# Kernel optimization log

Hardware: AMD Instinct MI355X
Metric: run time of the kernel (lower is better)

Reference implementation:

```python
import jax, jax.numpy as jnp
import numpy as np

N = 2048       # x_dim (input features)
M = 2048       # y_dim (output features)
R0 = 1024      # components in table 0 (knn table)
D_K = 1024     # key encoder embed dim
D_V = 1024     # val encoder embed dim
BATCH = 512
ISTA_ALPHA = 1.0
ISTA_MAXITER = 5


def _ortho_encoder(key, n, d):
    # get_embedding_matrix with ortho=True: QR of (s,s) gaussian, take [:n,:d]
    s = max(n, d)
    q = jnp.linalg.qr(jax.random.normal(key, (s, s), dtype=jnp.float32))[0]
    return q[:n, :d]


def setup_inputs() -> dict:
    key = jax.random.key(0)
    kw, kk, kv, kx = jax.random.split(key, 4)
    W = jax.random.normal(kw, (N, M), dtype=jnp.float32) / np.float32(np.sqrt(N))
    # torch: V, S, U = svd(W); U = U.T  -> V = left vecs (n,k), U = right vecs (m,k)
    Usvd, S, Vh = jnp.linalg.svd(W, full_matrices=False)
    V = Usvd          # (n, k)
    Ur = Vh.T         # (m, k)
    key_enc = _ortho_encoder(kk, N, D_K)   # (n, d_k)
    val_enc = _ortho_encoder(kv, M, D_V)   # (m, d_v)
    # table 0: knn table over components [0:R0]
    keys_t0 = V[:, :R0].T @ key_enc        # (R0, d_k)
    vals_t0 = Ur[:, :R0].T @ val_enc       # (R0, d_v)
    scales_t0 = S[:R0][:, None]            # (R0, 1)
    # table 1: plain low-rank table over components [R0:]
    keys_t1 = V[:, R0:]                    # (n, R1)
    vals_t1 = Ur[:, R0:]                   # (m, R1)
    scales_t1 = S[R0:][:, None]            # (R1, 1)
    x = jax.random.normal(kx, (BATCH, N), dtype=jnp.float32)
    return {"x": x, "key_enc": key_enc, "val_enc": val_enc,
            "keys_t0": keys_t0, "vals_t0": vals_t0, "scales_t0": scales_t0,
            "keys_t1": keys_t1, "vals_t1": vals_t1, "scales_t1": scales_t1}


def _soft(x, t):
    return jnp.sign(x) * jnp.maximum(jnp.abs(x) - t, 0.0)


def reference(x, key_enc, val_enc, keys_t0, vals_t0, scales_t0,
              keys_t1, vals_t1, scales_t1):
    # --- table 0: knn path (batched; original looped over batch samples) ---
    q = x @ key_enc                        # (B, d_k)
    alphas = q @ keys_t0.T                 # (B, R0)
    betas = alphas * scales_t0.T           # (B, R0)
    yb = betas @ vals_t0                   # (B, d_v)
    # ISTA: min ||yb - z @ val_enc||^2 + alpha*||z||_1, step=1 (val_enc has
    # orthonormal columns so Lipschitz const of grad is 1)
    z = yb @ val_enc.T                     # z0, (B, m)
    for _ in range(ISTA_MAXITER):
        z = _soft(z + (yb - z @ val_enc) @ val_enc.T, ISTA_ALPHA)
    y = z                                  # knn path assigns y[b,:] = yh
    # --- table 1: low-rank path (accumulates) ---
    alphas2 = x @ keys_t1                  # (B, R1)
    betas2 = alphas2 * scales_t1.T         # (B, R1)
    y = y + betas2 @ vals_t1.T             # (B, m)
    return y
```

## Files before the change

kernel.cpp:

```cpp
#include <hip/hip_runtime.h>


typedef _Float16 f16x8 __attribute__((ext_vector_type(8)));
typedef _Float16 f16x4 __attribute__((ext_vector_type(4)));
typedef float f32x4 __attribute__((ext_vector_type(4)));

enum { EPI_H, EPI_QOFF, EPI_SPLIT, EPI_SOFT, EPI_ZQ, EPI_ZQF, EPI_FINAL };

typedef const __attribute__((address_space(1))) void* gas_ptr;
typedef __attribute__((address_space(3))) void* las_ptr;

__device__ __forceinline__ void gload16(const void* g, void* l) {
  __builtin_amdgcn_global_load_lds((gas_ptr)g, (las_ptr)l, 16, 0, 0);
}

__device__ __forceinline__ float softt(float t) {
  float s = fabsf(t) - 1.0f;
  s = s > 0.0f ? s : 0.0f;
  return copysignf(s, t);
}

__global__ __launch_bounds__(256) void convAll(
    const float* __restrict__ e0, const float* __restrict__ e1,
    const float* __restrict__ e2, const float* __restrict__ e3,
    _Float16* __restrict__ o0, _Float16* __restrict__ o1,
    _Float16* __restrict__ o2, _Float16* __restrict__ o3,
    const float* __restrict__ s1, const float* __restrict__ s2,
    const float4* __restrict__ pa, f16x4* __restrict__ qa, int na,
    const float4* __restrict__ pb, f16x4* __restrict__ qb, int nb,
    const float4* __restrict__ pc, f16x4* __restrict__ qc, int nc) {
  const int z = blockIdx.z;
  if (z == 4) {
    const int total = na + nb + nc;
    const int bid = blockIdx.y * 32 + blockIdx.x;
    const int nthr = 2048 * 256;
    for (int i = bid * 256 + threadIdx.y * 32 + threadIdx.x; i < total;
         i += nthr) {
      const float4* s;
      f16x4* d;
      int j = i;
      if (j < na) {
        s = pa; d = qa;
      } else if ((j -= na) < nb) {
        s = pb; d = qb;
      } else {
        j -= nb; s = pc; d = qc;
      }
      float4 v = s[j];
      f16x4 h = {(_Float16)v.x, (_Float16)v.y, (_Float16)v.z, (_Float16)v.w};
      d[j] = h;
    }
    return;
  }
  const float* in = z == 0 ? e0 : z == 1 ? e1 : z == 2 ? e2 : e3;
  _Float16* out = z == 0 ? o0 : z == 1 ? o1 : z == 2 ? o2 : o3;
  const int R = (z < 2) ? 2048 : 1024;
  const int C = 1024;
  const int mode = z == 1 ? 1 : z == 2 ? 2 : 0;
  const float* sv = z == 1 ? s1 : s2;
  __shared__ float t[32][33];
  const int tx = threadIdx.x, ty = threadIdx.y;
  const int c0 = blockIdx.x * 32, r0 = blockIdx.y * 32;
  if (r0 >= R) return;
#pragma unroll
  for (int i = 0; i < 32; i += 8)
    t[ty + i][tx] = in[(size_t)(r0 + ty + i) * C + c0 + tx];
  __syncthreads();
#pragma unroll
  for (int i = 0; i < 32; i += 8) {
    float v = t[tx][ty + i];
    if (mode == 1) v *= sv[c0 + ty + i];
    if (mode == 2) v *= sv[r0 + tx];
    out[(size_t)(c0 + ty + i) * R + r0 + tx] = (_Float16)v;
  }
}

template <int EPI>
__device__ __forceinline__ void gtile(
    const _Float16* __restrict__ A, int lda, const _Float16* __restrict__ B,
    int ldb, int nK, int N, int brow, int bcol, const float* __restrict__ dgv,
    float* __restrict__ dgout, float* __restrict__ fA, float* __restrict__ fB,
    _Float16* __restrict__ oh, _Float16* __restrict__ oh2,
    float* __restrict__ ofin, _Float16* sm, int tid) {
  const int lane = tid & 63;
  const int w = tid >> 6;
  const int wr = w & 1;
  const int wk = w >> 1;
  const int srow = lane >> 3;
  const int scol = ((lane & 7) ^ srow) << 3;
  const int a15 = lane & 15;
  const int hi = lane >> 4;
  const int l7 = lane & 7;

  const _Float16* apg = A + (size_t)(brow + (w << 4) + srow) * lda + scol;
  const _Float16* bpg = B + (size_t)(bcol + (w << 4) + srow) * ldb + scol;
  _Float16* AB = sm;
  _Float16* BB = sm + 16384;
  const int ldstA = w << 10;

  const int ca = ((wk << 2) + hi) ^ l7;
  int raddr[2], baddr[4];
#pragma unroll
  for (int mi = 0; mi < 2; ++mi)
    raddr[mi] = ((wr << 5) + (mi << 4) + a15) * 64 + (ca << 3);
#pragma unroll
  for (int ni = 0; ni < 4; ++ni)
    baddr[ni] = ((ni << 4) + a15) * 64 + (ca << 3);

  f32x4 acc[2][4] = {};

  __syncthreads();

#pragma unroll
  for (int p = 0; p < 2; ++p) {
    gload16(apg + p * 64, AB + p * 4096 + ldstA);
    gload16(apg + p * 64 + (size_t)8 * lda, AB + p * 4096 + ldstA + 512);
    gload16(bpg + p * 64, BB + p * 4096 + ldstA);
    gload16(bpg + p * 64 + (size_t)8 * ldb, BB + p * 4096 + ldstA + 512);
  }

  for (int kt = 0; kt < nK; ++kt) {
    if (kt + 2 < nK) {
      const int bf = (kt + 2) & 3;
      const int co = (kt + 2) << 6;
      gload16(apg + co, AB + bf * 4096 + ldstA);
      gload16(apg + co + (size_t)8 * lda, AB + bf * 4096 + ldstA + 512);
      gload16(bpg + co, BB + bf * 4096 + ldstA);
      gload16(bpg + co + (size_t)8 * ldb, BB + bf * 4096 + ldstA + 512);
    }
    const int rem = nK - 1 - kt;
    if (rem >= 2)
      asm volatile("s_waitcnt vmcnt(8)" ::: "memory");
    else if (rem == 1)
      asm volatile("s_waitcnt vmcnt(4)" ::: "memory");
    else
      asm volatile("s_waitcnt vmcnt(0)" ::: "memory");
    __builtin_amdgcn_s_barrier();
    __builtin_amdgcn_sched_barrier(0);
    const _Float16* Ab = AB + (kt & 3) * 4096;
    const _Float16* Bb = BB + (kt & 3) * 4096;
    f16x8 av[2], bv[4];
    av[0] = *(const f16x8*)(Ab + raddr[0]);
    av[1] = *(const f16x8*)(Ab + raddr[1]);
    bv[0] = *(const f16x8*)(Bb + baddr[0]);
    bv[1] = *(const f16x8*)(Bb + baddr[1]);
    bv[2] = *(const f16x8*)(Bb + baddr[2]);
    bv[3] = *(const f16x8*)(Bb + baddr[3]);
#pragma unroll
    for (int mi = 0; mi < 2; ++mi)
#pragma unroll
      for (int ni = 0; ni < 4; ++ni)
        acc[mi][ni] = __builtin_amdgcn_mfma_f32_16x16x32_f16(
            av[mi], bv[ni], acc[mi][ni], 0, 0, 0);
  }

  __syncthreads();
  float* scr = (float*)sm;
  const int sl = (wr << 6) + lane;
  if (wk == 1) {
#pragma unroll
    for (int mi = 0; mi < 2; ++mi)
#pragma unroll
      for (int ni = 0; ni < 4; ++ni)
#pragma unroll
        for (int r = 0; r < 4; ++r)
          scr[(((mi << 2) + ni) * 4 + r) * 128 + sl] = acc[mi][ni][r];
  }
  __syncthreads();
  if (wk == 0) {
#pragma unroll
    for (int mi = 0; mi < 2; ++mi) {
#pragma unroll
      for (int ni = 0; ni < 4; ++ni) {
#pragma unroll
        for (int r = 0; r < 4; ++r) {
          const float v =
              acc[mi][ni][r] + scr[(((mi << 2) + ni) * 4 + r) * 128 + sl];
          const int row = brow + (wr << 5) + (mi << 4) + (hi << 2) + r;
          const int col = bcol + (ni << 4) + a15;
          const size_t idx = (size_t)row * N + col;
          if constexpr (EPI == EPI_H) {
            oh[idx] = (_Float16)v;
          } else if constexpr (EPI == EPI_QOFF) {
            if (row == col) {
              dgout[row] = 1.0f - v;
              oh[idx] = (_Float16)0.0f;
            } else {
              oh[idx] = (_Float16)(-v);
            }
          } else if constexpr (EPI == EPI_SPLIT) {
            if (col < 1024)
              oh[(size_t)row * 1024 + col] = (_Float16)v;
            else
              oh2[(size_t)row * 1024 + (col - 1024)] = (_Float16)v;
          }
        }
      }
    }
  }
}

template <int EPI>
__device__ __forceinline__ void gt32(
    const _Float16* __restrict__ A, int lda, const _Float16* __restrict__ B,
    int ldb, int nK, int N, int brow, int bcol, const float* __restrict__ dgv,
    float* __restrict__ fA, float* __restrict__ fB,
    _Float16* __restrict__ oh, float* __restrict__ ofin, _Float16* sm,
    int tid) {
  const int lane = tid & 63;
  const int w = tid >> 6;
  const int wc = w & 1;
  const int wk = w >> 1;
  const int srow = lane >> 3;
  const int scol = ((lane & 7) ^ srow) << 3;
  const int a15 = lane & 15, hi = lane >> 4, l7 = lane & 7;

  const _Float16* apg = A + (size_t)(brow + (w << 3) + srow) * lda + scol;
  const _Float16* bpg = B + (size_t)(bcol + (w << 4) + srow) * ldb + scol;
  _Float16* AB = sm;
  _Float16* BB = sm + 8192;
  const int ca = ((wk << 2) + hi) ^ l7;
  int raddr[2], baddr[2];
#pragma unroll
  for (int mi = 0; mi < 2; ++mi)
    raddr[mi] = ((mi << 4) + a15) * 64 + (ca << 3);
#pragma unroll
  for (int ni = 0; ni < 2; ++ni)
    baddr[ni] = ((wc << 5) + (ni << 4) + a15) * 64 + (ca << 3);

  f32x4 acc[2][2] = {};
  __syncthreads();

#pragma unroll
  for (int p = 0; p < 2; ++p) {
    gload16(apg + p * 64, AB + p * 2048 + (w << 9));
    gload16(bpg + p * 64, BB + p * 4096 + (w << 10));
    gload16(bpg + p * 64 + (size_t)8 * ldb, BB + p * 4096 + (w << 10) + 512);
  }
  for (int kt = 0; kt < nK; ++kt) {
    if (kt + 2 < nK) {
      const int bf = (kt + 2) & 3;
      const int co = (kt + 2) << 6;
      gload16(apg + co, AB + bf * 2048 + (w << 9));
      gload16(bpg + co, BB + bf * 4096 + (w << 10));
      gload16(bpg + co + (size_t)8 * ldb, BB + bf * 4096 + (w << 10) + 512);
    }
    const int rem = nK - 1 - kt;
    if (rem >= 2)
      asm volatile("s_waitcnt vmcnt(6)" ::: "memory");
    else if (rem == 1)
      asm volatile("s_waitcnt vmcnt(3)" ::: "memory");
    else
      asm volatile("s_waitcnt vmcnt(0)" ::: "memory");
    __builtin_amdgcn_s_barrier();
    __builtin_amdgcn_sched_barrier(0);
    const _Float16* Ab = AB + (kt & 3) * 2048;
    const _Float16* Bb = BB + (kt & 3) * 4096;
    f16x8 av[2], bv[2];
    av[0] = *(const f16x8*)(Ab + raddr[0]);
    av[1] = *(const f16x8*)(Ab + raddr[1]);
    bv[0] = *(const f16x8*)(Bb + baddr[0]);
    bv[1] = *(const f16x8*)(Bb + baddr[1]);
#pragma unroll
    for (int mi = 0; mi < 2; ++mi)
#pragma unroll
      for (int ni = 0; ni < 2; ++ni)
        acc[mi][ni] = __builtin_amdgcn_mfma_f32_16x16x32_f16(
            av[mi], bv[ni], acc[mi][ni], 0, 0, 0);
  }
  __syncthreads();
  float* scr = (float*)sm;
  const int sl = (wc << 6) + lane;
  if (wk == 1) {
#pragma unroll
    for (int mi = 0; mi < 2; ++mi)
#pragma unroll
      for (int ni = 0; ni < 2; ++ni)
#pragma unroll
        for (int r = 0; r < 4; ++r)
          scr[(((mi << 1) + ni) * 4 + r) * 128 + sl] = acc[mi][ni][r];
  }
  __syncthreads();
  if (wk == 0) {
#pragma unroll
    for (int mi = 0; mi < 2; ++mi) {
#pragma unroll
      for (int ni = 0; ni < 2; ++ni) {
#pragma unroll
        for (int r = 0; r < 4; ++r) {
          const float v =
              acc[mi][ni][r] + scr[(((mi << 1) + ni) * 4 + r) * 128 + sl];
          const int row = brow + (mi << 4) + (hi << 2) + r;
          const int col = bcol + (wc << 5) + (ni << 4) + a15;
          const size_t idx = (size_t)row * N + col;
          if constexpr (EPI == EPI_SOFT) {
            fA[idx] = v;
            float s = softt(v);
            fB[idx] = s;
            oh[idx] = (_Float16)s;
          } else if constexpr (EPI == EPI_ZQ) {
            float t = fA[idx] + dgv[col] * fB[idx] + v;
            float s = softt(t);
            fB[idx] = s;
            oh[idx] = (_Float16)s;
          } else if constexpr (EPI == EPI_ZQF) {
            float t = fA[idx] + dgv[col] * fB[idx] + v;
            fB[idx] = softt(t);
          } else {
            ofin[idx] = fB[idx] + v;
          }
        }
      }
    }
  }
}

struct WS {
  const _Float16 *ve, *vt1, *w0pT_r, *Bcat, *qoff_r, *x, *kt0s, *vt0T, *w0_r,
      *q_r, *be2;
  _Float16 *w0pT_w, *qoff_w, *w0_w, *q_w, *be2_w, *zhA, *zhB;
  float *z0, *zf, *dg;
};

__device__ __forceinline__ void map512(int b, int& br, int& bc) {
  const int x = b & 7, i = b >> 3;
  bc = (x << 2) | (i & 3);
  br = i >> 2;
}

__global__ __launch_bounds__(256, 2) void kD2(WS p) {
  __shared__ __align__(16) _Float16 sm[32768];
  const int tid = threadIdx.x;
  const int bid = blockIdx.x;
  if (bid < 1024) {
    gtile<EPI_QOFF>(p.ve, 1024, p.ve, 1024, 16, 2048, (bid >> 5) << 6,
                    (bid & 31) << 6, nullptr, p.dg, nullptr, nullptr, p.qoff_w,
                    nullptr, nullptr, sm, tid);
  } else if (bid < 1280) {
    const int i = bid - 1024;
    gtile<EPI_SPLIT>(p.x, 2048, p.Bcat, 2048, 32, 2048, (i >> 5) << 6,
                     (i & 31) << 6, nullptr, nullptr, nullptr, nullptr, p.q_w,
                     p.be2_w, nullptr, sm, tid);
  } else {
    const int i = bid - 1280;
    gtile<EPI_H>(p.kt0s, 1024, p.vt0T, 1024, 16, 1024, (i >> 4) << 6,
                 (i & 15) << 6, nullptr, nullptr, nullptr, nullptr, p.w0_w,
                 nullptr, nullptr, sm, tid);
  }
}

__global__ __launch_bounds__(256, 2) void kW0p(WS p) {
  __shared__ __align__(16) _Float16 sm[32768];
  const int x = blockIdx.x & 7, i = blockIdx.x >> 3;
  const int bc = (x << 1) | (i & 1), br = i >> 1;
  gtile<EPI_H>(p.ve, 1024, p.w0_r, 1024, 16, 1024, br << 6, bc << 6, nullptr,
               nullptr, nullptr, nullptr, p.w0pT_w, nullptr, nullptr, sm,
               threadIdx.x);
}

__global__ __launch_bounds__(256, 2) void kC2(WS p) {
  __shared__ __align__(16) _Float16 sm[24576];
  int br, bc;
  map512(blockIdx.x, br, bc);
  gt32<EPI_SOFT>(p.q_r, 1024, p.w0pT_r, 1024, 16, 2048, br << 5, bc << 6,
                 nullptr, p.z0, p.zf, p.zhA, nullptr, sm, threadIdx.x);
}

template <bool AB>
__global__ __launch_bounds__(256, 2) void kZQ(WS p) {
  __shared__ __align__(16) _Float16 sm[24576];
  int br, bc;
  map512(blockIdx.x, br, bc);
  gt32<EPI_ZQ>(AB ? p.zhA : p.zhB, 2048, p.qoff_r, 2048, 32, 2048, br << 5,
               bc << 6, p.dg, p.z0, p.zf, AB ? p.zhB : p.zhA, nullptr, sm,
               threadIdx.x);
}

__global__ __launch_bounds__(256, 2) void kZQF(WS p, float* out) {
  __shared__ __align__(16) _Float16 sm[24576];
  int br, bc;
  map512(blockIdx.x, br, bc);
  gt32<EPI_ZQF>(p.zhB, 2048, p.qoff_r, 2048, 32, 2048, br << 5, bc << 6, p.dg,
                p.z0, p.zf, nullptr, nullptr, sm, threadIdx.x);
  gt32<EPI_FINAL>(p.be2, 1024, p.vt1, 1024, 16, 2048, br << 5, bc << 6,
                  nullptr, nullptr, p.zf, nullptr, out, sm, threadIdx.x);
}

extern "C" void kernel_launch(void* const* d_in, const int* in_sizes, int n_in,
                              void* d_out, int out_size, void* d_ws,
                              size_t ws_size, hipStream_t stream) {
  const float* x = (const float*)d_in[0];
  const float* key_enc = (const float*)d_in[1];
  const float* val_enc = (const float*)d_in[2];
  const float* keys_t0 = (const float*)d_in[3];
  const float* vals_t0 = (const float*)d_in[4];
  const float* scales_t0 = (const float*)d_in[5];
  const float* keys_t1 = (const float*)d_in[6];
  const float* vals_t1 = (const float*)d_in[7];
  const float* scales_t1 = (const float*)d_in[8];

  constexpr size_t M1 = 1048576;
  _Float16* ws = (_Float16*)d_ws;
  _Float16* ve_h = ws;
  _Float16* vt1_h = ws + 2 * M1;
  _Float16* w0pT = ws + 4 * M1;
  _Float16* Bcat = ws + 6 * M1;
  _Float16* zhA = ws + 6 * M1;
  float* z0_f = (float*)(ws + 7 * M1);
  _Float16* zhB = ws + 9 * M1;
  _Float16* qoff = ws + 10 * M1;
  _Float16* x_h = ws + 14 * M1;
  _Float16* kt0s = ws + 15 * M1;
  float* z_f = (float*)(ws + 15 * M1);
  _Float16* vt0T = ws + 16 * M1;
  _Float16* w0 = ws + 17 * M1;
  _Float16* q_h = ws + 18 * M1;
  _Float16* be2 = ws + 18 * M1 + 524288;
  float* dg = (float*)(ws + 19 * M1);

  WS p;
  p.ve = ve_h; p.vt1 = vt1_h; p.w0pT_r = w0pT; p.w0pT_w = w0pT;
  p.Bcat = Bcat; p.qoff_r = qoff; p.qoff_w = qoff; p.x = x_h;
  p.kt0s = kt0s; p.vt0T = vt0T; p.w0_r = w0; p.w0_w = w0;
  p.q_r = q_h; p.q_w = q_h; p.be2 = be2; p.be2_w = be2;
  p.zhA = zhA; p.zhB = zhB; p.z0 = z0_f; p.zf = z_f; p.dg = dg;

  convAll<<<dim3(32, 64, 5), dim3(32, 8), 0, stream>>>(
      key_enc, keys_t1, keys_t0, vals_t0, Bcat, Bcat + 2 * M1, kt0s, vt0T,
      scales_t1, scales_t0, (const float4*)x, (f16x4*)x_h, 262144,
      (const float4*)val_enc, (f16x4*)ve_h, 524288, (const float4*)vals_t1,
      (f16x4*)vt1_h, 524288);
  kD2<<<1536, 256, 0, stream>>>(p);
  kW0p<<<512, 256, 0, stream>>>(p);
  kC2<<<512, 256, 0, stream>>>(p);
  kZQ<true><<<512, 256, 0, stream>>>(p);
  kZQ<false><<<512, 256, 0, stream>>>(p);
  kZQ<true><<<512, 256, 0, stream>>>(p);
  kZQF<<<512, 256, 0, stream>>>(p, (float*)d_out);
}
```

Baseline: 110.3 us.

## Reassociate knn-table GEMM chain and deepen gt32 pipeline to three stages

```diff
diff --git a/kernel.cpp b/kernel.cpp
--- a/kernel.cpp
+++ b/kernel.cpp
@@ -21,67 +21,64 @@
 }
 
 __global__ __launch_bounds__(256) void convAll(
-    const float* __restrict__ e0, const float* __restrict__ e1,
-    const float* __restrict__ e2, const float* __restrict__ e3,
-    _Float16* __restrict__ o0, _Float16* __restrict__ o1,
-    _Float16* __restrict__ o2, _Float16* __restrict__ o3,
-    const float* __restrict__ s1, const float* __restrict__ s2,
-    const float4* __restrict__ pa, f16x4* __restrict__ qa, int na,
-    const float4* __restrict__ pb, f16x4* __restrict__ qb, int nb,
-    const float4* __restrict__ pc, f16x4* __restrict__ qc, int nc) {
-  const int z = blockIdx.z;
-  if (z == 4) {
-    const int total = na + nb + nc;
-    const int bid = blockIdx.y * 32 + blockIdx.x;
-    const int nthr = 2048 * 256;
-    for (int i = bid * 256 + threadIdx.y * 32 + threadIdx.x; i < total;
-         i += nthr) {
-      const float4* s;
-      f16x4* d;
-      int j = i;
-      if (j < na) {
-        s = pa; d = qa;
-      } else if ((j -= na) < nb) {
-        s = pb; d = qb;
-      } else {
-        j -= nb; s = pc; d = qc;
-      }
-      float4 v = s[j];
-      f16x4 h = {(_Float16)v.x, (_Float16)v.y, (_Float16)v.z, (_Float16)v.w};
-      d[j] = h;
+    const float* __restrict__ k1, _Float16* __restrict__ k1s1T,
+    const float* __restrict__ s1, const float* __restrict__ x,
+    _Float16* __restrict__ x_h, const float* __restrict__ ve,
+    _Float16* __restrict__ ve_h, const float* __restrict__ vt1,
+    _Float16* __restrict__ vt1_h, const float* __restrict__ k0,
+    _Float16* __restrict__ k0s, const float* __restrict__ s0,
+    const float* __restrict__ v0, _Float16* __restrict__ v0_h,
+    const float* __restrict__ ke, _Float16* __restrict__ ke_h) {
+  if (blockIdx.z == 0) {
+    __shared__ float t[32][33];
+    const int tx = threadIdx.x, ty = threadIdx.y;
+    const int c0 = blockIdx.x * 32, r0 = blockIdx.y * 32;
+#pragma unroll
+    for (int i = 0; i < 32; i += 8)
+      t[ty + i][tx] = k1[(size_t)(r0 + ty + i) * 1024 + c0 + tx];
+    __syncthreads();
+#pragma unroll
+    for (int i = 0; i < 32; i += 8) {
+      float v = t[tx][ty + i] * s1[c0 + ty + i];
+      k1s1T[(size_t)(c0 + ty + i) * 2048 + r0 + tx] = (_Float16)v;
     }
     return;
   }
-  const float* in = z == 0 ? e0 : z == 1 ? e1 : z == 2 ? e2 : e3;
-  _Float16* out = z == 0 ? o0 : z == 1 ? o1 : z == 2 ? o2 : o3;
-  const int R = (z < 2) ? 2048 : 1024;
-  const int C = 1024;
-  const int mode = z == 1 ? 1 : z == 2 ? 2 : 0;
-  const float* sv = z == 1 ? s1 : s2;
-  __shared__ float t[32][33];
-  const int tx = threadIdx.x, ty = threadIdx.y;
-  const int c0 = blockIdx.x * 32, r0 = blockIdx.y * 32;
-  if (r0 >= R) return;
-#pragma unroll
-  for (int i = 0; i < 32; i += 8)
-    t[ty + i][tx] = in[(size_t)(r0 + ty + i) * C + c0 + tx];
-  __syncthreads();
-#pragma unroll
-  for (int i = 0; i < 32; i += 8) {
-    float v = t[tx][ty + i];
-    if (mode == 1) v *= sv[c0 + ty + i];
-    if (mode == 2) v *= sv[r0 + tx];
-    out[(size_t)(c0 + ty + i) * R + r0 + tx] = (_Float16)v;
+  const int bid = blockIdx.y * 32 + blockIdx.x;
+  const int n_x = 262144, n_ve = 524288, n_v1 = 524288, n_k0 = 262144,
+            n_v0 = 262144, n_ke = 524288;
+  const int total = n_x + n_ve + n_v1 + n_k0 + n_v0 + n_ke;
+  for (int i = bid * 256 + threadIdx.y * 32 + threadIdx.x; i < total;
+       i += 2048 * 256) {
+    int j = i;
+    const float4* s;
+    f16x4* d;
+    float sc = 1.0f;
+    if (j < n_x) {
+      s = (const float4*)x; d = (f16x4*)x_h;
+    } else if ((j -= n_x) < n_ve) {
+      s = (const float4*)ve; d = (f16x4*)ve_h;
+    } else if ((j -= n_ve) < n_v1) {
+      s = (const float4*)vt1; d = (f16x4*)vt1_h;
+    } else if ((j -= n_v1) < n_k0) {
+      s = (const float4*)k0; d = (f16x4*)k0s; sc = s0[j >> 8];
+    } else if ((j -= n_k0) < n_v0) {
+      s = (const float4*)v0; d = (f16x4*)v0_h;
+    } else {
+      j -= n_v0; s = (const float4*)ke; d = (f16x4*)ke_h;
+    }
+    float4 v = s[j];
+    f16x4 h = {(_Float16)(v.x * sc), (_Float16)(v.y * sc),
+               (_Float16)(v.z * sc), (_Float16)(v.w * sc)};
+    d[j] = h;
   }
 }
 
 template <int EPI>
 __device__ __forceinline__ void gtile(
     const _Float16* __restrict__ A, int lda, const _Float16* __restrict__ B,
-    int ldb, int nK, int N, int brow, int bcol, const float* __restrict__ dgv,
-    float* __restrict__ dgout, float* __restrict__ fA, float* __restrict__ fB,
-    _Float16* __restrict__ oh, _Float16* __restrict__ oh2,
-    float* __restrict__ ofin, _Float16* sm, int tid) {
+    int ldb, int nK, int N, int brow, int bcol, float* __restrict__ dgout,
+    _Float16* __restrict__ oh, _Float16* sm, int tid) {
   const int lane = tid & 63;
   const int w = tid >> 6;
   const int wr = w & 1;
@@ -181,18 +178,13 @@
           const size_t idx = (size_t)row * N + col;
           if constexpr (EPI == EPI_H) {
             oh[idx] = (_Float16)v;
-          } else if constexpr (EPI == EPI_QOFF) {
+          } else {
             if (row == col) {
               dgout[row] = 1.0f - v;
               oh[idx] = (_Float16)0.0f;
             } else {
               oh[idx] = (_Float16)(-v);
             }
-          } else if constexpr (EPI == EPI_SPLIT) {
-            if (col < 1024)
-              oh[(size_t)row * 1024 + col] = (_Float16)v;
-            else
-              oh2[(size_t)row * 1024 + (col - 1024)] = (_Float16)v;
           }
         }
       }
@@ -205,8 +197,8 @@
     const _Float16* __restrict__ A, int lda, const _Float16* __restrict__ B,
     int ldb, int nK, int N, int brow, int bcol, const float* __restrict__ dgv,
     float* __restrict__ fA, float* __restrict__ fB,
-    _Float16* __restrict__ oh, float* __restrict__ ofin, _Float16* sm,
-    int tid) {
+    _Float16* __restrict__ oh, _Float16* __restrict__ oh2,
+    float* __restrict__ ofin, _Float16* sm, int tid) {
   const int lane = tid & 63;
   const int w = tid >> 6;
   const int wc = w & 1;
@@ -218,7 +210,7 @@
   const _Float16* apg = A + (size_t)(brow + (w << 3) + srow) * lda + scol;
   const _Float16* bpg = B + (size_t)(bcol + (w << 4) + srow) * ldb + scol;
   _Float16* AB = sm;
-  _Float16* BB = sm + 8192;
+  _Float16* BB = sm + 10240;
   const int ca = ((wk << 2) + hi) ^ l7;
   int raddr[2], baddr[2];
 #pragma unroll
@@ -232,21 +224,23 @@
   __syncthreads();
 
 #pragma unroll
-  for (int p = 0; p < 2; ++p) {
+  for (int p = 0; p < 3; ++p) {
     gload16(apg + p * 64, AB + p * 2048 + (w << 9));
     gload16(bpg + p * 64, BB + p * 4096 + (w << 10));
     gload16(bpg + p * 64 + (size_t)8 * ldb, BB + p * 4096 + (w << 10) + 512);
   }
+  int bi = 0, bs = 3;
   for (int kt = 0; kt < nK; ++kt) {
-    if (kt + 2 < nK) {
-      const int bf = (kt + 2) & 3;
-      const int co = (kt + 2) << 6;
-      gload16(apg + co, AB + bf * 2048 + (w << 9));
-      gload16(bpg + co, BB + bf * 4096 + (w << 10));
-      gload16(bpg + co + (size_t)8 * ldb, BB + bf * 4096 + (w << 10) + 512);
+    if (kt + 3 < nK) {
+      const int co = (kt + 3) << 6;
+      gload16(apg + co, AB + bs * 2048 + (w << 9));
+      gload16(bpg + co, BB + bs * 4096 + (w << 10));
+      gload16(bpg + co + (size_t)8 * ldb, BB + bs * 4096 + (w << 10) + 512);
     }
     const int rem = nK - 1 - kt;
-    if (rem >= 2)
+    if (rem >= 3)
+      asm volatile("s_waitcnt vmcnt(9)" ::: "memory");
+    else if (rem == 2)
       asm volatile("s_waitcnt vmcnt(6)" ::: "memory");
     else if (rem == 1)
       asm volatile("s_waitcnt vmcnt(3)" ::: "memory");
@@ -254,8 +248,8 @@
       asm volatile("s_waitcnt vmcnt(0)" ::: "memory");
     __builtin_amdgcn_s_barrier();
     __builtin_amdgcn_sched_barrier(0);
-    const _Float16* Ab = AB + (kt & 3) * 2048;
-    const _Float16* Bb = BB + (kt & 3) * 4096;
+    const _Float16* Ab = AB + bi * 2048;
+    const _Float16* Bb = BB + bi * 4096;
     f16x8 av[2], bv[2];
     av[0] = *(const f16x8*)(Ab + raddr[0]);
     av[1] = *(const f16x8*)(Ab + raddr[1]);
@@ -267,6 +261,8 @@
       for (int ni = 0; ni < 2; ++ni)
         acc[mi][ni] = __builtin_amdgcn_mfma_f32_16x16x32_f16(
             av[mi], bv[ni], acc[mi][ni], 0, 0, 0);
+    bi = bi == 4 ? 0 : bi + 1;
+    bs = bs == 4 ? 0 : bs + 1;
   }
   __syncthreads();
   float* scr = (float*)sm;
@@ -293,7 +289,12 @@
           const int row = brow + (mi << 4) + (hi << 2) + r;
           const int col = bcol + (wc << 5) + (ni << 4) + a15;
           const size_t idx = (size_t)row * N + col;
-          if constexpr (EPI == EPI_SOFT) {
+          if constexpr (EPI == EPI_SPLIT) {
+            if (col < 1024)
+              oh[(size_t)row * 1024 + col] = (_Float16)v;
+            else
+              oh2[(size_t)row * 1024 + (col - 1024)] = (_Float16)v;
+          } else if constexpr (EPI == EPI_SOFT) {
             fA[idx] = v;
             float s = softt(v);
             fB[idx] = s;
@@ -316,9 +317,9 @@
 }
 
 struct WS {
-  const _Float16 *ve, *vt1, *w0pT_r, *Bcat, *qoff_r, *x, *kt0s, *vt0T, *w0_r,
-      *q_r, *be2;
-  _Float16 *w0pT_w, *qoff_w, *w0_w, *q_w, *be2_w, *zhA, *zhB;
+  const _Float16 *ve, *vt1, *w1T_r, *Bcat, *qoff_r, *x, *k0s, *v0, *ke,
+      *bet_r, *be2_r;
+  _Float16 *w1T_w, *KbT_w, *qoff_w, *bet_w, *be2_w, *zhA, *zhB;
   float *z0, *zf, *dg;
 };
 
@@ -334,56 +335,55 @@
   const int bid = blockIdx.x;
   if (bid < 1024) {
     gtile<EPI_QOFF>(p.ve, 1024, p.ve, 1024, 16, 2048, (bid >> 5) << 6,
-                    (bid & 31) << 6, nullptr, p.dg, nullptr, nullptr, p.qoff_w,
-                    nullptr, nullptr, sm, tid);
-  } else if (bid < 1280) {
+                    (bid & 31) << 6, p.dg, p.qoff_w, sm, tid);
+  } else if (bid < 1536) {
     const int i = bid - 1024;
-    gtile<EPI_SPLIT>(p.x, 2048, p.Bcat, 2048, 32, 2048, (i >> 5) << 6,
-                     (i & 31) << 6, nullptr, nullptr, nullptr, nullptr, p.q_w,
-                     p.be2_w, nullptr, sm, tid);
+    gtile<EPI_H>(p.k0s, 1024, p.ke, 1024, 16, 2048, (i >> 5) << 6,
+                 (i & 31) << 6, nullptr, p.KbT_w, sm, tid);
   } else {
-    const int i = bid - 1280;
-    gtile<EPI_H>(p.kt0s, 1024, p.vt0T, 1024, 16, 1024, (i >> 4) << 6,
-                 (i & 15) << 6, nullptr, nullptr, nullptr, nullptr, p.w0_w,
-                 nullptr, nullptr, sm, tid);
-  }
-}
-
-__global__ __launch_bounds__(256, 2) void kW0p(WS p) {
-  __shared__ __align__(16) _Float16 sm[32768];
-  const int x = blockIdx.x & 7, i = blockIdx.x >> 3;
-  const int bc = (x << 1) | (i & 1), br = i >> 1;
-  gtile<EPI_H>(p.ve, 1024, p.w0_r, 1024, 16, 1024, br << 6, bc << 6, nullptr,
-               nullptr, nullptr, nullptr, p.w0pT_w, nullptr, nullptr, sm,
-               threadIdx.x);
-}
-
-__global__ __launch_bounds__(256, 2) void kC2(WS p) {
-  __shared__ __align__(16) _Float16 sm[24576];
+    const int i = bid - 1536;
+    gtile<EPI_H>(p.ve, 1024, p.v0, 1024, 16, 1024, (i >> 4) << 6,
+                 (i & 15) << 6, nullptr, p.w1T_w, sm, tid);
+  }
+}
+
+__global__ __launch_bounds__(256, 2) void kC1(WS p) {
+  __shared__ __align__(16) _Float16 sm[30720];
   int br, bc;
   map512(blockIdx.x, br, bc);
-  gt32<EPI_SOFT>(p.q_r, 1024, p.w0pT_r, 1024, 16, 2048, br << 5, bc << 6,
-                 nullptr, p.z0, p.zf, p.zhA, nullptr, sm, threadIdx.x);
+  gt32<EPI_SPLIT>(p.x, 2048, p.Bcat, 2048, 32, 2048, br << 5, bc << 6,
+                  nullptr, nullptr, nullptr, p.bet_w, p.be2_w, nullptr, sm,
+                  threadIdx.x);
+}
+
+__global__ __launch_bounds__(256, 2) void kC2(WS p) {
+  __shared__ __align__(16) _Float16 sm[30720];
+  int br, bc;
+  map512(blockIdx.x, br, bc);
+  gt32<EPI_SOFT>(p.bet_r, 1024, p.w1T_r, 1024, 16, 2048, br << 5, bc << 6,
+                 nullptr, p.z0, p.zf, p.zhA, nullptr, nullptr, sm,
+                 threadIdx.x);
 }
 
 template <bool AB>
 __global__ __launch_bounds__(256, 2) void kZQ(WS p) {
-  __shared__ __align__(16) _Float16 sm[24576];
+  __shared__ __align__(16) _Float16 sm[30720];
   int br, bc;
   map512(blockIdx.x, br, bc);
   gt32<EPI_ZQ>(AB ? p.zhA : p.zhB, 2048, p.qoff_r, 2048, 32, 2048, br << 5,
-               bc << 6, p.dg, p.z0, p.zf, AB ? p.zhB : p.zhA, nullptr, sm,
-               threadIdx.x);
+               bc << 6, p.dg, p.z0, p.zf, AB ? p.zhB : p.zhA, nullptr,
+               nullptr, sm, threadIdx.x);
 }
 
 __global__ __launch_bounds__(256, 2) void kZQF(WS p, float* out) {
-  __shared__ __align__(16) _Float16 sm[24576];
+  __shared__ __align__(16) _Float16 sm[30720];
   int br, bc;
   map512(blockIdx.x, br, bc);
   gt32<EPI_ZQF>(p.zhB, 2048, p.qoff_r, 2048, 32, 2048, br << 5, bc << 6, p.dg,
-                p.z0, p.zf, nullptr, nullptr, sm, threadIdx.x);
-  gt32<EPI_FINAL>(p.be2, 1024, p.vt1, 1024, 16, 2048, br << 5, bc << 6,
-                  nullptr, nullptr, p.zf, nullptr, out, sm, threadIdx.x);
+                p.z0, p.zf, nullptr, nullptr, nullptr, sm, threadIdx.x);
+  gt32<EPI_FINAL>(p.be2_r, 1024, p.vt1, 1024, 16, 2048, br << 5, bc << 6,
+                  nullptr, nullptr, p.zf, nullptr, nullptr, out, sm,
+                  threadIdx.x);
 }
 
 extern "C" void kernel_launch(void* const* d_in, const int* in_sizes, int n_in,
@@ -402,36 +402,34 @@
   constexpr size_t M1 = 1048576;
   _Float16* ws = (_Float16*)d_ws;
   _Float16* ve_h = ws;
+  float* z_f = (float*)ws;
   _Float16* vt1_h = ws + 2 * M1;
-  _Float16* w0pT = ws + 4 * M1;
+  _Float16* w1T = ws + 4 * M1;
   _Float16* Bcat = ws + 6 * M1;
   _Float16* zhA = ws + 6 * M1;
-  float* z0_f = (float*)(ws + 7 * M1);
-  _Float16* zhB = ws + 9 * M1;
-  _Float16* qoff = ws + 10 * M1;
-  _Float16* x_h = ws + 14 * M1;
-  _Float16* kt0s = ws + 15 * M1;
-  float* z_f = (float*)(ws + 15 * M1);
-  _Float16* vt0T = ws + 16 * M1;
-  _Float16* w0 = ws + 17 * M1;
-  _Float16* q_h = ws + 18 * M1;
-  _Float16* be2 = ws + 18 * M1 + 524288;
-  float* dg = (float*)(ws + 19 * M1);
+  _Float16* zhB = ws + 7 * M1;
+  float* z0_f = (float*)(ws + 8 * M1);
+  _Float16* ke_h = ws + 10 * M1;
+  _Float16* x_h = ws + 12 * M1;
+  _Float16* k0s = ws + 13 * M1;
+  _Float16* bet_h = ws + 13 * M1;
+  _Float16* be2_h = ws + 13 * M1 + 524288;
+  _Float16* v0_h = ws + 14 * M1;
+  float* dg = (float*)(ws + 15 * M1);
+  _Float16* qoff = ws + 16 * M1;
 
   WS p;
-  p.ve = ve_h; p.vt1 = vt1_h; p.w0pT_r = w0pT; p.w0pT_w = w0pT;
-  p.Bcat = Bcat; p.qoff_r = qoff; p.qoff_w = qoff; p.x = x_h;
-  p.kt0s = kt0s; p.vt0T = vt0T; p.w0_r = w0; p.w0_w = w0;
-  p.q_r = q_h; p.q_w = q_h; p.be2 = be2; p.be2_w = be2;
+  p.ve = ve_h; p.vt1 = vt1_h; p.w1T_r = w1T; p.w1T_w = w1T;
+  p.Bcat = Bcat; p.KbT_w = Bcat; p.qoff_r = qoff; p.qoff_w = qoff;
+  p.x = x_h; p.k0s = k0s; p.v0 = v0_h; p.ke = ke_h;
+  p.bet_r = bet_h; p.bet_w = bet_h; p.be2_r = be2_h; p.be2_w = be2_h;
   p.zhA = zhA; p.zhB = zhB; p.z0 = z0_f; p.zf = z_f; p.dg = dg;
 
-  convAll<<<dim3(32, 64, 5), dim3(32, 8), 0, stream>>>(
-      key_enc, keys_t1, keys_t0, vals_t0, Bcat, Bcat + 2 * M1, kt0s, vt0T,
-      scales_t1, scales_t0, (const float4*)x, (f16x4*)x_h, 262144,
-      (const float4*)val_enc, (f16x4*)ve_h, 524288, (const float4*)vals_t1,
-      (f16x4*)vt1_h, 524288);
-  kD2<<<1536, 256, 0, stream>>>(p);
-  kW0p<<<512, 256, 0, stream>>>(p);
+  convAll<<<dim3(32, 64, 2), dim3(32, 8), 0, stream>>>(
+      keys_t1, Bcat + 2 * M1, scales_t1, x, x_h, val_enc, ve_h, vals_t1,
+      vt1_h, keys_t0, k0s, scales_t0, vals_t0, v0_h, key_enc, ke_h);
+  kD2<<<2048, 256, 0, stream>>>(p);
+  kC1<<<512, 256, 0, stream>>>(p);
   kC2<<<512, 256, 0, stream>>>(p);
   kZQ<true><<<512, 256, 0, stream>>>(p);
   kZQ<false><<<512, 256, 0, stream>>>(p);
```

Measured after the change: 117.4 us. +6.5%, slower.

## Move low-rank table GEMM into the first ISTA kernel launch

Applied to the files above, without the earlier changes.

```diff
diff --git a/kernel.cpp b/kernel.cpp
--- a/kernel.cpp
+++ b/kernel.cpp
@@ -5,7 +5,7 @@
 typedef _Float16 f16x4 __attribute__((ext_vector_type(4)));
 typedef float f32x4 __attribute__((ext_vector_type(4)));
 
-enum { EPI_H, EPI_QOFF, EPI_SPLIT, EPI_SOFT, EPI_ZQ, EPI_ZQF, EPI_FINAL };
+enum { EPI_H, EPI_QOFF, EPI_SPLIT, EPI_SOFT, EPI_YP, EPI_ZQ, EPI_ZQFO };
 
 typedef const __attribute__((address_space(1))) void* gas_ptr;
 typedef __attribute__((address_space(3))) void* las_ptr;
@@ -78,10 +78,9 @@
 template <int EPI>
 __device__ __forceinline__ void gtile(
     const _Float16* __restrict__ A, int lda, const _Float16* __restrict__ B,
-    int ldb, int nK, int N, int brow, int bcol, const float* __restrict__ dgv,
-    float* __restrict__ dgout, float* __restrict__ fA, float* __restrict__ fB,
-    _Float16* __restrict__ oh, _Float16* __restrict__ oh2,
-    float* __restrict__ ofin, _Float16* sm, int tid) {
+    int ldb, int nK, int N, int brow, int bcol, float* __restrict__ dgout,
+    _Float16* __restrict__ oh, _Float16* __restrict__ oh2, _Float16* sm,
+    int tid) {
   const int lane = tid & 63;
   const int w = tid >> 6;
   const int wr = w & 1;
@@ -188,7 +187,7 @@
             } else {
               oh[idx] = (_Float16)(-v);
             }
-          } else if constexpr (EPI == EPI_SPLIT) {
+          } else {
             if (col < 1024)
               oh[(size_t)row * 1024 + col] = (_Float16)v;
             else
@@ -205,8 +204,8 @@
     const _Float16* __restrict__ A, int lda, const _Float16* __restrict__ B,
     int ldb, int nK, int N, int brow, int bcol, const float* __restrict__ dgv,
     float* __restrict__ fA, float* __restrict__ fB,
-    _Float16* __restrict__ oh, float* __restrict__ ofin, _Float16* sm,
-    int tid) {
+    _Float16* __restrict__ oh, const float* __restrict__ fC,
+    float* __restrict__ ofin, _Float16* sm, int tid) {
   const int lane = tid & 63;
   const int w = tid >> 6;
   const int wc = w & 1;
@@ -298,16 +297,16 @@
             float s = softt(v);
             fB[idx] = s;
             oh[idx] = (_Float16)s;
+          } else if constexpr (EPI == EPI_YP) {
+            ofin[idx] = v;
           } else if constexpr (EPI == EPI_ZQ) {
             float t = fA[idx] + dgv[col] * fB[idx] + v;
             float s = softt(t);
             fB[idx] = s;
             oh[idx] = (_Float16)s;
-          } else if constexpr (EPI == EPI_ZQF) {
+          } else {
             float t = fA[idx] + dgv[col] * fB[idx] + v;
-            fB[idx] = softt(t);
-          } else {
-            ofin[idx] = fB[idx] + v;
+            ofin[idx] = fC[idx] + softt(t);
           }
         }
       }
@@ -319,7 +318,7 @@
   const _Float16 *ve, *vt1, *w0pT_r, *Bcat, *qoff_r, *x, *kt0s, *vt0T, *w0_r,
       *q_r, *be2;
   _Float16 *w0pT_w, *qoff_w, *w0_w, *q_w, *be2_w, *zhA, *zhB;
-  float *z0, *zf, *dg;
+  float *z0, *zf, *dg, *yp;
 };
 
 __device__ __forceinline__ void map512(int b, int& br, int& bc) {
@@ -334,18 +333,15 @@
   const int bid = blockIdx.x;
   if (bid < 1024) {
     gtile<EPI_QOFF>(p.ve, 1024, p.ve, 1024, 16, 2048, (bid >> 5) << 6,
-                    (bid & 31) << 6, nullptr, p.dg, nullptr, nullptr, p.qoff_w,
-                    nullptr, nullptr, sm, tid);
+                    (bid & 31) << 6, p.dg, p.qoff_w, nullptr, sm, tid);
   } else if (bid < 1280) {
     const int i = bid - 1024;
     gtile<EPI_SPLIT>(p.x, 2048, p.Bcat, 2048, 32, 2048, (i >> 5) << 6,
-                     (i & 31) << 6, nullptr, nullptr, nullptr, nullptr, p.q_w,
-                     p.be2_w, nullptr, sm, tid);
+                     (i & 31) << 6, nullptr, p.q_w, p.be2_w, sm, tid);
   } else {
     const int i = bid - 1280;
     gtile<EPI_H>(p.kt0s, 1024, p.vt0T, 1024, 16, 1024, (i >> 4) << 6,
-                 (i & 15) << 6, nullptr, nullptr, nullptr, nullptr, p.w0_w,
-                 nullptr, nullptr, sm, tid);
+                 (i & 15) << 6, nullptr, p.w0_w, nullptr, sm, tid);
   }
 }
 
@@ -354,16 +350,24 @@
   const int x = blockIdx.x & 7, i = blockIdx.x >> 3;
   const int bc = (x << 1) | (i & 1), br = i >> 1;
   gtile<EPI_H>(p.ve, 1024, p.w0_r, 1024, 16, 1024, br << 6, bc << 6, nullptr,
-               nullptr, nullptr, nullptr, p.w0pT_w, nullptr, nullptr, sm,
-               threadIdx.x);
-}
-
-__global__ __launch_bounds__(256, 2) void kC2(WS p) {
+               p.w0pT_w, nullptr, sm, threadIdx.x);
+}
+
+__global__ __launch_bounds__(256, 3) void kD4(WS p) {
   __shared__ __align__(16) _Float16 sm[24576];
+  const int bid = blockIdx.x;
   int br, bc;
-  map512(blockIdx.x, br, bc);
-  gt32<EPI_SOFT>(p.q_r, 1024, p.w0pT_r, 1024, 16, 2048, br << 5, bc << 6,
-                 nullptr, p.z0, p.zf, p.zhA, nullptr, sm, threadIdx.x);
+  if (bid < 512) {
+    map512(bid, br, bc);
+    gt32<EPI_SOFT>(p.q_r, 1024, p.w0pT_r, 1024, 16, 2048, br << 5, bc << 6,
+                   nullptr, p.z0, p.zf, p.zhA, nullptr, nullptr, sm,
+                   threadIdx.x);
+  } else {
+    map512(bid - 512, br, bc);
+    gt32<EPI_YP>(p.be2, 1024, p.vt1, 1024, 16, 2048, br << 5, bc << 6,
+                 nullptr, nullptr, nullptr, nullptr, nullptr, p.yp, sm,
+                 threadIdx.x);
+  }
 }
 
 template <bool AB>
@@ -372,18 +376,16 @@
   int br, bc;
   map512(blockIdx.x, br, bc);
   gt32<EPI_ZQ>(AB ? p.zhA : p.zhB, 2048, p.qoff_r, 2048, 32, 2048, br << 5,
-               bc << 6, p.dg, p.z0, p.zf, AB ? p.zhB : p.zhA, nullptr, sm,
-               threadIdx.x);
+               bc << 6, p.dg, p.z0, p.zf, AB ? p.zhB : p.zhA, nullptr,
+               nullptr, sm, threadIdx.x);
 }
 
 __global__ __launch_bounds__(256, 2) void kZQF(WS p, float* out) {
   __shared__ __align__(16) _Float16 sm[24576];
   int br, bc;
   map512(blockIdx.x, br, bc);
-  gt32<EPI_ZQF>(p.zhB, 2048, p.qoff_r, 2048, 32, 2048, br << 5, bc << 6, p.dg,
-                p.z0, p.zf, nullptr, nullptr, sm, threadIdx.x);
-  gt32<EPI_FINAL>(p.be2, 1024, p.vt1, 1024, 16, 2048, br << 5, bc << 6,
-                  nullptr, nullptr, p.zf, nullptr, out, sm, threadIdx.x);
+  gt32<EPI_ZQFO>(p.zhB, 2048, p.qoff_r, 2048, 32, 2048, br << 5, bc << 6,
+                 p.dg, p.z0, p.zf, nullptr, p.yp, out, sm, threadIdx.x);
 }
 
 extern "C" void kernel_launch(void* const* d_in, const int* in_sizes, int n_in,
@@ -402,6 +404,7 @@
   constexpr size_t M1 = 1048576;
   _Float16* ws = (_Float16*)d_ws;
   _Float16* ve_h = ws;
+  float* yp = (float*)ws;
   _Float16* vt1_h = ws + 2 * M1;
   _Float16* w0pT = ws + 4 * M1;
   _Float16* Bcat = ws + 6 * M1;
@@ -423,7 +426,7 @@
   p.Bcat = Bcat; p.qoff_r = qoff; p.qoff_w = qoff; p.x = x_h;
   p.kt0s = kt0s; p.vt0T = vt0T; p.w0_r = w0; p.w0_w = w0;
   p.q_r = q_h; p.q_w = q_h; p.be2 = be2; p.be2_w = be2;
-  p.zhA = zhA; p.zhB = zhB; p.z0 = z0_f; p.zf = z_f; p.dg = dg;
+  p.zhA = zhA; p.zhB = zhB; p.z0 = z0_f; p.zf = z_f; p.dg = dg; p.yp = yp;
 
   convAll<<<dim3(32, 64, 5), dim3(32, 8), 0, stream>>>(
       key_enc, keys_t1, keys_t0, vals_t0, Bcat, Bcat + 2 * M1, kt0s, vt0T,
@@ -432,7 +435,7 @@
       (f16x4*)vt1_h, 524288);
   kD2<<<1536, 256, 0, stream>>>(p);
   kW0p<<<512, 256, 0, stream>>>(p);
-  kC2<<<512, 256, 0, stream>>>(p);
+  kD4<<<1024, 256, 0, stream>>>(p);
   kZQ<true><<<512, 256, 0, stream>>>(p);
   kZQ<false><<<512, 256, 0, stream>>>(p);
   kZQ<true><<<512, 256, 0, stream>>>(p);
```

New measurement: 110.3 us, median of 2. About the same (-0.0%).
